# Optimization experiments

Measured on AMD Instinct MI355X. Metric: run time of the kernel, lower is better.

## Reference

```python
import jax, jax.numpy as jnp
import numpy as np

N_CELL, N_GENE, D, E = 100000, 20000, 128, 1000000


def setup_inputs() -> dict:
    key = jax.random.key(0)
    ks = jax.random.split(key, 16)
    return {
        "cell_z": jax.random.normal(ks[0], (N_CELL, D), jnp.float32),
        "gene_z": jax.random.normal(ks[1], (N_GENE, D), jnp.float32),
        "W_gene": jax.random.normal(ks[2], (D, D), jnp.float32) / np.sqrt(D),
        "b_gene": jax.random.normal(ks[3], (D,), jnp.float32) * 0.01,
        "cell_scale": jax.random.normal(ks[4], (N_CELL,), jnp.float32),
        "cell_bias": jax.random.normal(ks[5], (N_CELL,), jnp.float32),
        "cell_std": jax.random.uniform(ks[6], (N_CELL,), jnp.float32, 0.1, 1.0),
        "gene_scale": jax.random.normal(ks[7], (N_GENE,), jnp.float32),
        "gene_bias": jax.random.normal(ks[8], (N_GENE,), jnp.float32),
        "gene_std": jax.random.uniform(ks[9], (N_GENE,), jnp.float32, 0.1, 1.0),
        "src_idx": jax.random.randint(ks[10], (E,), 0, N_CELL, jnp.int32),
        "dst_idx": jax.random.randint(ks[11], (E,), 0, N_GENE, jnp.int32),
        "cell_n_id": jax.random.randint(ks[12], (N_CELL,), 0, N_CELL, jnp.int32),
        "gene_n_id": jax.random.randint(ks[13], (N_GENE,), 0, N_GENE, jnp.int32),
    }


def reference(cell_z, gene_z, W_gene, b_gene,
              cell_scale, cell_bias, cell_std,
              gene_scale, gene_bias, gene_std,
              src_idx, dst_idx, cell_n_id, gene_n_id):
    # Relation projection: 'cell' -> Identity, 'gene' -> Linear + LeakyReLU.
    # Project per-node then gather (mathematically identical to the original
    # gather-then-project since projection is pointwise per node).
    gene_proj = jax.nn.leaky_relu(gene_z @ W_gene + b_gene)  # [N_GENE, D]
    u = cell_z[src_idx]            # [E, D] gather of src node embeddings
    v = gene_proj[dst_idx]         # [E, D] gather of projected dst embeddings

    # Per-edge scale/bias/std lookups via global node ids (n_id[edge_index]).
    sid = cell_n_id[src_idx]       # [E]
    did = gene_n_id[dst_idx]       # [E]
    s_sc, s_b, s_sd = cell_scale[sid], cell_bias[sid], cell_std[sid]
    d_sc, d_b, d_sd = gene_scale[did], gene_bias[did], gene_std[did]

    dot = jnp.sum(u * v, axis=-1)  # [E]
    loc = dot * s_sc * d_sc + s_b + d_b
    std = s_sd * d_sd
    return jnp.stack([loc, std])   # [2, E]
```

## Files before the change

kernel.cpp:

```cpp
#include <hip/hip_runtime.h>

#define N_CELL 100000
#define N_GENE 20000
#define DIM    128
#define N_EDGE 1000000

#define NS_STRIPE 15
#define NTILE     45
#define NBLK_SORT 977

#define NB_CAST 6250
#define NB_HIST 977
#define NB_PROJ 1250
#define NB_CTAB 391
#define NB_GTAB 79
#define NB_PREP (NB_CAST + NB_HIST + NB_PROJ + NB_CTAB + NB_GTAB)

typedef float f32x4 __attribute__((ext_vector_type(4)));

__device__ inline unsigned short f2bf(float f) {
    unsigned u = __float_as_uint(f);
    u += 0x7fffu + ((u >> 16) & 1u);
    return (unsigned short)(u >> 16);
}

__device__ inline void dot2(float& acc, unsigned a, unsigned b) {
    asm("v_dot2_f32_bf16 %0, %1, %2, %0" : "+v"(acc) : "v"(a), "v"(b));
}

__device__ inline int tile_of(int s, int d) {
    const int ss = (int)(((long long)s * 161049LL) >> 30);
    const int ds = (int)(((long long)d * 161049LL) >> 30);
    return ds * NS_STRIPE + ss;
}

__global__ __launch_bounds__(256) void prep_kernel(
    const float* __restrict__ gene_z,
    const float* __restrict__ W,
    const float* __restrict__ b,
    ushort* __restrict__ gene_projb,
    const float* __restrict__ cell_z,
    ushort4* __restrict__ cell_zb4,
    const int*   __restrict__ src_idx,
    const int*   __restrict__ dst_idx,
    const int*   __restrict__ cell_n_id,
    const int*   __restrict__ gene_n_id,
    const float* __restrict__ cell_scale,
    const float* __restrict__ cell_bias,
    const float* __restrict__ cell_std,
    const float* __restrict__ gene_scale,
    const float* __restrict__ gene_bias,
    const float* __restrict__ gene_std,
    float4* __restrict__ cell_p4,
    float4* __restrict__ gene_p4,
    int* __restrict__ counts)
{
    __shared__ float zlds[16][DIM];

    const int tid = threadIdx.x;
    int blk = blockIdx.x;

    if (blk < NB_CAST) {
        const f32x4* in4 = (const f32x4*)cell_z;
        const int base = blk * 512 + tid;
        const f32x4 v0 = __builtin_nontemporal_load(in4 + base);
        const f32x4 v1 = __builtin_nontemporal_load(in4 + base + 256);
        ushort4 o0, o1;
        o0.x = f2bf(v0.x); o0.y = f2bf(v0.y); o0.z = f2bf(v0.z); o0.w = f2bf(v0.w);
        o1.x = f2bf(v1.x); o1.y = f2bf(v1.y); o1.z = f2bf(v1.z); o1.w = f2bf(v1.w);
        cell_zb4[base]       = o0;
        cell_zb4[base + 256] = o1;
        return;
    }
    blk -= NB_CAST;

    if (blk < NB_HIST) {
        if (!counts) return;
        int* lcnt = (int*)&zlds[0][0];
        if (tid < NTILE) lcnt[tid] = 0;
        __syncthreads();
        #pragma unroll
        for (int c = 0; c < 4; ++c) {
            const int e = blk * 1024 + c * 256 + tid;
            if (e < N_EDGE) {
                const int t = tile_of(src_idx[e], dst_idx[e]);
                atomicAdd(&lcnt[t], 1);
            }
        }
        __syncthreads();
        if (tid < NTILE) counts[tid * NBLK_SORT + blk] = lcnt[tid];
        return;
    }
    blk -= NB_HIST;

    if (blk < NB_PROJ) {
        const int row0 = blk * 16;
        const f32x4* Z4  = (const f32x4*)(gene_z + (long)row0 * DIM);
        f32x4*       zl4 = (f32x4*)&zlds[0][0];
        zl4[tid]       = __builtin_nontemporal_load(Z4 + tid);
        zl4[tid + 256] = __builtin_nontemporal_load(Z4 + tid + 256);
        __syncthreads();

        const int col   = tid & 127;
        const int rbase = (tid >> 7) * 8;

        const float bias = b[col];
        float acc[8];
        #pragma unroll
        for (int r = 0; r < 8; ++r) acc[r] = bias;

        #pragma unroll 8
        for (int k4 = 0; k4 < DIM / 4; ++k4) {
            float4 zv[8];
            #pragma unroll
            for (int r = 0; r < 8; ++r)
                zv[r] = ((const float4*)&zlds[rbase + r][0])[k4];
            #pragma unroll
            for (int kk = 0; kk < 4; ++kk) {
                const float w = W[(k4 * 4 + kk) * DIM + col];
                #pragma unroll
                for (int r = 0; r < 8; ++r) {
                    const float z = (kk == 0) ? zv[r].x : (kk == 1) ? zv[r].y
                                   : (kk == 2) ? zv[r].z : zv[r].w;
                    acc[r] = fmaf(z, w, acc[r]);
                }
            }
        }
        #pragma unroll
        for (int r = 0; r < 8; ++r) {
            const float v = acc[r];
            gene_projb[(long)(row0 + rbase + r) * DIM + col] =
                f2bf(v > 0.f ? v : 0.01f * v);
        }
        return;
    }
    blk -= NB_PROJ;

    if (blk < NB_CTAB) {
        if (!cell_p4) return;
        const int c = blk * 256 + tid;
        if (c < N_CELL) {
            const int id = cell_n_id[c];
            cell_p4[c] = make_float4(cell_scale[id], cell_bias[id],
                                     cell_std[id], 0.f);
        }
        return;
    }
    blk -= NB_CTAB;

    if (!gene_p4) return;
    const int g = blk * 256 + tid;
    if (g < N_GENE) {
        const int id = gene_n_id[g];
        gene_p4[g] = make_float4(gene_scale[id], gene_bias[id],
                                 gene_std[id], 0.f);
    }
}

__global__ __launch_bounds__(256) void scanA_kernel(
    int* __restrict__ counts, int* __restrict__ totals)
{
    __shared__ int sd[256];
    const int t   = blockIdx.x;
    const int tid = threadIdx.x;
    int carry = 0;
    for (int c = 0; c < 4; ++c) {
        const int idx = c * 256 + tid;
        const int val = (idx < NBLK_SORT) ? counts[t * NBLK_SORT + idx] : 0;
        sd[tid] = val;
        __syncthreads();
        #pragma unroll
        for (int off = 1; off < 256; off <<= 1) {
            const int tmp = (tid >= off) ? sd[tid - off] : 0;
            __syncthreads();
            sd[tid] += tmp;
            __syncthreads();
        }
        const int incl  = sd[tid];
        const int ctot  = sd[255];
        if (idx < NBLK_SORT) counts[t * NBLK_SORT + idx] = carry + incl - val;
        carry += ctot;
        __syncthreads();
    }
    if (tid == 0) totals[t] = carry;
}

__global__ void scanB_kernel(const int* __restrict__ totals,
                             int* __restrict__ bases)
{
    if (threadIdx.x == 0 && blockIdx.x == 0) {
        int s = 0;
        for (int i = 0; i < NTILE; ++i) { bases[i] = s; s += totals[i]; }
    }
}

__global__ __launch_bounds__(256) void scatter_kernel(
    const int* __restrict__ src_idx,
    const int* __restrict__ dst_idx,
    const int* __restrict__ counts,
    const int* __restrict__ bases,
    int2* __restrict__ sorted_sd,
    int*  __restrict__ sorted_e)
{
    __shared__ int lcnt[NTILE];
    __shared__ int lbase[NTILE];
    const int tid = threadIdx.x;
    const int blk = blockIdx.x;
    if (tid < NTILE) lcnt[tid] = 0;
    __syncthreads();

    int ts[4], rs[4], ss[4], ds[4], es[4];
    #pragma unroll
    for (int c = 0; c < 4; ++c) {
        const int e = blk * 1024 + c * 256 + tid;
        es[c] = e;
        if (e < N_EDGE) {
            ss[c] = src_idx[e];
            ds[c] = dst_idx[e];
            ts[c] = tile_of(ss[c], ds[c]);
            rs[c] = atomicAdd(&lcnt[ts[c]], 1);
        } else { ts[c] = -1; rs[c] = 0; ss[c] = 0; ds[c] = 0; }
    }
    __syncthreads();
    if (tid < NTILE) lbase[tid] = bases[tid] + counts[tid * NBLK_SORT + blk];
    __syncthreads();

    #pragma unroll
    for (int c = 0; c < 4; ++c) {
        if (ts[c] >= 0) {
            const int pos = lbase[ts[c]] + rs[c];
            sorted_sd[pos] = make_int2(ss[c], ds[c]);
            sorted_e[pos]  = es[c];
        }
    }
}

__global__ __launch_bounds__(256) void edge_sorted_kernel(
    const ushort* __restrict__ cell_zb,
    const ushort* __restrict__ gene_projb,
    const int2* __restrict__ sorted_sd,
    const int*  __restrict__ sorted_e,
    const float4* __restrict__ cell_p4,
    const float4* __restrict__ gene_p4,
    float* __restrict__ out)
{
    const int wg  = blockIdx.x;
    const int xcd = wg & 7;
    const int sub = wg >> 3;
    const int q = 15625 / 8, r = 15625 % 8;
    const int swz = ((xcd < r) ? xcd * (q + 1) : r * (q + 1) + (xcd - r) * q) + sub;

    const int tid  = threadIdx.x;
    const int lane = tid & 15;
    const int grp  = swz * 16 + (tid >> 4);

    const int4 p0 = ((const int4*)sorted_sd)[grp * 2];
    const int4 p1 = ((const int4*)sorted_sd)[grp * 2 + 1];
    const int4 e4 = ((const int4*)sorted_e)[grp];

    uint4 a0 = ((const uint4*)(cell_zb    + (long)p0.x * DIM))[lane];
    uint4 a1 = ((const uint4*)(cell_zb    + (long)p0.z * DIM))[lane];
    uint4 a2 = ((const uint4*)(cell_zb    + (long)p1.x * DIM))[lane];
    uint4 a3 = ((const uint4*)(cell_zb    + (long)p1.z * DIM))[lane];
    uint4 v0 = ((const uint4*)(gene_projb + (long)p0.y * DIM))[lane];
    uint4 v1 = ((const uint4*)(gene_projb + (long)p0.w * DIM))[lane];
    uint4 v2 = ((const uint4*)(gene_projb + (long)p1.y * DIM))[lane];
    uint4 v3 = ((const uint4*)(gene_projb + (long)p1.w * DIM))[lane];

    float dot0 = 0.f, dot1 = 0.f, dot2v = 0.f, dot3 = 0.f;
    dot2(dot0, a0.x, v0.x); dot2(dot0, a0.y, v0.y);
    dot2(dot0, a0.z, v0.z); dot2(dot0, a0.w, v0.w);
    dot2(dot1, a1.x, v1.x); dot2(dot1, a1.y, v1.y);
    dot2(dot1, a1.z, v1.z); dot2(dot1, a1.w, v1.w);
    dot2(dot2v, a2.x, v2.x); dot2(dot2v, a2.y, v2.y);
    dot2(dot2v, a2.z, v2.z); dot2(dot2v, a2.w, v2.w);
    dot2(dot3, a3.x, v3.x); dot2(dot3, a3.y, v3.y);
    dot2(dot3, a3.z, v3.z); dot2(dot3, a3.w, v3.w);

    #define RED(d)                 \
        d += __shfl_xor(d, 1);     \
        d += __shfl_xor(d, 2);     \
        d += __shfl_xor(d, 4);     \
        d += __shfl_xor(d, 8);
    RED(dot0) RED(dot1) RED(dot2v) RED(dot3)
    #undef RED

    if (lane < 4) {
        const float dj = (lane & 2) ? ((lane & 1) ? dot3 : dot2v)
                                    : ((lane & 1) ? dot1 : dot0);
        const int sj   = (lane & 2) ? ((lane & 1) ? p1.z : p1.x)
                                    : ((lane & 1) ? p0.z : p0.x);
        const int djx  = (lane & 2) ? ((lane & 1) ? p1.w : p1.y)
                                    : ((lane & 1) ? p0.w : p0.y);
        const int e    = (lane & 2) ? ((lane & 1) ? e4.w : e4.z)
                                    : ((lane & 1) ? e4.y : e4.x);
        const float4 cs = cell_p4[sj];
        const float4 gs = gene_p4[djx];
        out[e]          = dj * cs.x * gs.x + cs.y + gs.y;
        out[N_EDGE + e] = cs.z * gs.z;
    }
}

template<bool TAB>
__global__ __launch_bounds__(256) void edge_kernel(
    const ushort* __restrict__ cell_zb,
    const ushort* __restrict__ gene_projb,
    const int*   __restrict__ src_idx,
    const int*   __restrict__ dst_idx,
    const int*   __restrict__ cell_n_id,
    const int*   __restrict__ gene_n_id,
    const float* __restrict__ cell_scale,
    const float* __restrict__ cell_bias,
    const float* __restrict__ cell_std,
    const float* __restrict__ gene_scale,
    const float* __restrict__ gene_bias,
    const float* __restrict__ gene_std,
    const float4* __restrict__ cell_p4,
    const float4* __restrict__ gene_p4,
    float* __restrict__ out)
{
    const int tid  = threadIdx.x;
    const int lane = tid & 15;
    const int grp  = blockIdx.x * 16 + (tid >> 4);
    const int e0   = grp * 4;

    const int4 s4 = ((const int4*)src_idx)[grp];
    const int4 d4 = ((const int4*)dst_idx)[grp];

    uint4 a0 = ((const uint4*)(cell_zb    + (long)s4.x * DIM))[lane];
    uint4 a1 = ((const uint4*)(cell_zb    + (long)s4.y * DIM))[lane];
    uint4 a2 = ((const uint4*)(cell_zb    + (long)s4.z * DIM))[lane];
    uint4 a3 = ((const uint4*)(cell_zb    + (long)s4.w * DIM))[lane];
    uint4 v0 = ((const uint4*)(gene_projb + (long)d4.x * DIM))[lane];
    uint4 v1 = ((const uint4*)(gene_projb + (long)d4.y * DIM))[lane];
    uint4 v2 = ((const uint4*)(gene_projb + (long)d4.z * DIM))[lane];
    uint4 v3 = ((const uint4*)(gene_projb + (long)d4.w * DIM))[lane];

    float dot0 = 0.f, dot1 = 0.f, dot2v = 0.f, dot3 = 0.f;
    dot2(dot0, a0.x, v0.x); dot2(dot0, a0.y, v0.y);
    dot2(dot0, a0.z, v0.z); dot2(dot0, a0.w, v0.w);
    dot2(dot1, a1.x, v1.x); dot2(dot1, a1.y, v1.y);
    dot2(dot1, a1.z, v1.z); dot2(dot1, a1.w, v1.w);
    dot2(dot2v, a2.x, v2.x); dot2(dot2v, a2.y, v2.y);
    dot2(dot2v, a2.z, v2.z); dot2(dot2v, a2.w, v2.w);
    dot2(dot3, a3.x, v3.x); dot2(dot3, a3.y, v3.y);
    dot2(dot3, a3.z, v3.z); dot2(dot3, a3.w, v3.w);

    #define RED(d)                 \
        d += __shfl_xor(d, 1);     \
        d += __shfl_xor(d, 2);     \
        d += __shfl_xor(d, 4);     \
        d += __shfl_xor(d, 8);
    RED(dot0) RED(dot1) RED(dot2v) RED(dot3)
    #undef RED

    if (lane < 4) {
        const float dj = (lane & 2) ? ((lane & 1) ? dot3 : dot2v)
                                    : ((lane & 1) ? dot1 : dot0);
        const int sj   = (lane & 2) ? ((lane & 1) ? s4.w : s4.z)
                                    : ((lane & 1) ? s4.y : s4.x);
        const int djx  = (lane & 2) ? ((lane & 1) ? d4.w : d4.z)
                                    : ((lane & 1) ? d4.y : d4.x);
        float sc_s, b_s, sd_s, sc_d, b_d, sd_d;
        if (TAB) {
            const float4 cs = cell_p4[sj];
            const float4 gs = gene_p4[djx];
            sc_s = cs.x; b_s = cs.y; sd_s = cs.z;
            sc_d = gs.x; b_d = gs.y; sd_d = gs.z;
        } else {
            const int sid = cell_n_id[sj];
            const int did = gene_n_id[djx];
            sc_s = cell_scale[sid]; b_s = cell_bias[sid]; sd_s = cell_std[sid];
            sc_d = gene_scale[did]; b_d = gene_bias[did]; sd_d = gene_std[did];
        }
        const int e = e0 + lane;
        out[e]          = dj * sc_s * sc_d + b_s + b_d;
        out[N_EDGE + e] = sd_s * sd_d;
    }
}

extern "C" void kernel_launch(void* const* d_in, const int* in_sizes, int n_in,
                              void* d_out, int out_size, void* d_ws, size_t ws_size,
                              hipStream_t stream) {
    const float* cell_z     = (const float*)d_in[0];
    const float* gene_z     = (const float*)d_in[1];
    const float* W_gene     = (const float*)d_in[2];
    const float* b_gene     = (const float*)d_in[3];
    const float* cell_scale = (const float*)d_in[4];
    const float* cell_bias  = (const float*)d_in[5];
    const float* cell_std   = (const float*)d_in[6];
    const float* gene_scale = (const float*)d_in[7];
    const float* gene_bias  = (const float*)d_in[8];
    const float* gene_std   = (const float*)d_in[9];
    const int*   src_idx    = (const int*)d_in[10];
    const int*   dst_idx    = (const int*)d_in[11];
    const int*   cell_n_id  = (const int*)d_in[12];
    const int*   gene_n_id  = (const int*)d_in[13];

    char* ws = (char*)d_ws;
    size_t off = 0;
    ushort* gene_projb = (ushort*)(ws + off); off += (size_t)N_GENE * DIM * 2;
    ushort* cell_zb    = (ushort*)(ws + off); off += (size_t)N_CELL * DIM * 2;
    const size_t base_need = off;

    float4* cell_p4 = nullptr; float4* gene_p4 = nullptr;
    size_t off_tab = off;
    const size_t tab_need = (size_t)N_CELL * 16 + (size_t)N_GENE * 16;

    int2* sorted_sd = nullptr; int* sorted_e = nullptr;
    int* counts = nullptr; int* totals = nullptr; int* bases = nullptr;

    const size_t sort_need = (size_t)N_EDGE * 8 + (size_t)N_EDGE * 4
                           + (size_t)NTILE * NBLK_SORT * 4 + 512;

    const bool tab  = (ws_size >= base_need + tab_need);
    const bool srt  = tab && (ws_size >= base_need + tab_need + sort_need);

    if (tab) {
        cell_p4 = (float4*)(ws + off_tab);
        gene_p4 = (float4*)(ws + off_tab + (size_t)N_CELL * 16);
        off = off_tab + tab_need;
    }
    if (srt) {
        sorted_sd = (int2*)(ws + off); off += (size_t)N_EDGE * 8;
        sorted_e  = (int*)(ws + off);  off += (size_t)N_EDGE * 4;
        counts    = (int*)(ws + off);  off += (size_t)NTILE * NBLK_SORT * 4;
        totals    = (int*)(ws + off);  off += 256;
        bases     = (int*)(ws + off);  off += 256;
    }

    float* out = (float*)d_out;

    prep_kernel<<<NB_PREP, 256, 0, stream>>>(
        gene_z, W_gene, b_gene, gene_projb,
        cell_z, (ushort4*)cell_zb,
        src_idx, dst_idx, cell_n_id, gene_n_id,
        cell_scale, cell_bias, cell_std,
        gene_scale, gene_bias, gene_std,
        cell_p4, gene_p4, counts);

    if (srt) {
        scanA_kernel<<<NTILE, 256, 0, stream>>>(counts, totals);
        scanB_kernel<<<1, 64, 0, stream>>>(totals, bases);
        scatter_kernel<<<NBLK_SORT, 256, 0, stream>>>(
            src_idx, dst_idx, counts, bases, sorted_sd, sorted_e);
        edge_sorted_kernel<<<N_EDGE / 64, 256, 0, stream>>>(
            cell_zb, gene_projb, sorted_sd, sorted_e, cell_p4, gene_p4, out);
    } else if (tab) {
        edge_kernel<true><<<N_EDGE / 64, 256, 0, stream>>>(
            cell_zb, gene_projb, src_idx, dst_idx, cell_n_id, gene_n_id,
            cell_scale, cell_bias, cell_std, gene_scale, gene_bias, gene_std,
            cell_p4, gene_p4, out);
    } else {
        edge_kernel<false><<<N_EDGE / 64, 256, 0, stream>>>(
            cell_zb, gene_projb, src_idx, dst_idx, cell_n_id, gene_n_id,
            cell_scale, cell_bias, cell_std, gene_scale, gene_bias, gene_std,
            nullptr, nullptr, out);
    }
}
```

Measured before the change: 107.1 us.

## Pack sorted edge indices, write results in sorted order, add gather fixup pass

Edges are now bucketed into 20 source stripes by 2 destination halves, and each edge's source and destination are packed into one 32-bit word, which halves the sorted-index traffic. The edge kernel writes float2 results in sorted order, and a new fixup kernel gathers them back to original edge order through a rank array, so the output stores become coalesced. The one-thread base scan kernel is folded into the scatter kernel, removing a launch. The projection loop is restructured, and nontemporal loads are replaced with normal loads. In exchange there is an extra kernel launch plus an intermediate result buffer that is written and then read back with random gathers.

```diff
diff --git a/kernel.cpp b/kernel.cpp
--- a/kernel.cpp
+++ b/kernel.cpp
@@ -5,8 +5,9 @@
 #define DIM    128
 #define N_EDGE 1000000
 
-#define NS_STRIPE 15
-#define NTILE     45
+#define NS_STRIPE 20
+#define ND_STRIPE 2
+#define NTILE     40
 #define NBLK_SORT 977
 
 #define NB_CAST 6250
@@ -29,9 +30,13 @@
 }
 
 __device__ inline int tile_of(int s, int d) {
-    const int ss = (int)(((long long)s * 161049LL) >> 30);
-    const int ds = (int)(((long long)d * 161049LL) >> 30);
+    const int ss = (int)(((unsigned long long)s * 429497ULL) >> 31);
+    const int ds = (d >= 10000) ? 1 : 0;
     return ds * NS_STRIPE + ss;
+}
+
+__device__ inline unsigned pack_sd(int s, int d) {
+    return ((unsigned)s << 15) | (unsigned)d;
 }
 
 __global__ __launch_bounds__(256) void prep_kernel(
@@ -63,8 +68,8 @@
     if (blk < NB_CAST) {
         const f32x4* in4 = (const f32x4*)cell_z;
         const int base = blk * 512 + tid;
-        const f32x4 v0 = __builtin_nontemporal_load(in4 + base);
-        const f32x4 v1 = __builtin_nontemporal_load(in4 + base + 256);
+        const f32x4 v0 = in4[base];
+        const f32x4 v1 = in4[base + 256];
         ushort4 o0, o1;
         o0.x = f2bf(v0.x); o0.y = f2bf(v0.y); o0.z = f2bf(v0.z); o0.w = f2bf(v0.w);
         o1.x = f2bf(v1.x); o1.y = f2bf(v1.y); o1.z = f2bf(v1.z); o1.w = f2bf(v1.w);
@@ -97,8 +102,8 @@
         const int row0 = blk * 16;
         const f32x4* Z4  = (const f32x4*)(gene_z + (long)row0 * DIM);
         f32x4*       zl4 = (f32x4*)&zlds[0][0];
-        zl4[tid]       = __builtin_nontemporal_load(Z4 + tid);
-        zl4[tid + 256] = __builtin_nontemporal_load(Z4 + tid + 256);
+        zl4[tid]       = Z4[tid];
+        zl4[tid + 256] = Z4[tid + 256];
         __syncthreads();
 
         const int col   = tid & 127;
@@ -109,21 +114,19 @@
         #pragma unroll
         for (int r = 0; r < 8; ++r) acc[r] = bias;
 
-        #pragma unroll 8
         for (int k4 = 0; k4 < DIM / 4; ++k4) {
-            float4 zv[8];
+            const float w0 = W[(k4 * 4 + 0) * DIM + col];
+            const float w1 = W[(k4 * 4 + 1) * DIM + col];
+            const float w2 = W[(k4 * 4 + 2) * DIM + col];
+            const float w3 = W[(k4 * 4 + 3) * DIM + col];
             #pragma unroll
-            for (int r = 0; r < 8; ++r)
-                zv[r] = ((const float4*)&zlds[rbase + r][0])[k4];
-            #pragma unroll
-            for (int kk = 0; kk < 4; ++kk) {
-                const float w = W[(k4 * 4 + kk) * DIM + col];
-                #pragma unroll
-                for (int r = 0; r < 8; ++r) {
-                    const float z = (kk == 0) ? zv[r].x : (kk == 1) ? zv[r].y
-                                   : (kk == 2) ? zv[r].z : zv[r].w;
-                    acc[r] = fmaf(z, w, acc[r]);
-                }
+            for (int rp = 0; rp < 4; ++rp) {
+                const float4 za = ((const float4*)&zlds[rbase + 2*rp][0])[k4];
+                const float4 zb = ((const float4*)&zlds[rbase + 2*rp + 1][0])[k4];
+                acc[2*rp]     = fmaf(za.x, w0, fmaf(za.y, w1,
+                                fmaf(za.z, w2, fmaf(za.w, w3, acc[2*rp]))));
+                acc[2*rp + 1] = fmaf(zb.x, w0, fmaf(zb.y, w1,
+                                fmaf(zb.z, w2, fmaf(zb.w, w3, acc[2*rp + 1]))));
             }
         }
         #pragma unroll
@@ -176,44 +179,35 @@
             sd[tid] += tmp;
             __syncthreads();
         }
-        const int incl  = sd[tid];
-        const int ctot  = sd[255];
+        const int incl = sd[tid];
+        const int ctot = sd[255];
         if (idx < NBLK_SORT) counts[t * NBLK_SORT + idx] = carry + incl - val;
         carry += ctot;
         __syncthreads();
     }
     if (tid == 0) totals[t] = carry;
-}
-
-__global__ void scanB_kernel(const int* __restrict__ totals,
-                             int* __restrict__ bases)
-{
-    if (threadIdx.x == 0 && blockIdx.x == 0) {
-        int s = 0;
-        for (int i = 0; i < NTILE; ++i) { bases[i] = s; s += totals[i]; }
-    }
 }
 
 __global__ __launch_bounds__(256) void scatter_kernel(
     const int* __restrict__ src_idx,
     const int* __restrict__ dst_idx,
     const int* __restrict__ counts,
-    const int* __restrict__ bases,
-    int2* __restrict__ sorted_sd,
-    int*  __restrict__ sorted_e)
+    const int* __restrict__ totals,
+    unsigned* __restrict__ sorted_p,
+    int*      __restrict__ rank)
 {
     __shared__ int lcnt[NTILE];
+    __shared__ int sbase[NTILE];
     __shared__ int lbase[NTILE];
     const int tid = threadIdx.x;
     const int blk = blockIdx.x;
     if (tid < NTILE) lcnt[tid] = 0;
     __syncthreads();
 
-    int ts[4], rs[4], ss[4], ds[4], es[4];
+    int ts[4], rs[4], ss[4], ds[4];
     #pragma unroll
     for (int c = 0; c < 4; ++c) {
         const int e = blk * 1024 + c * 256 + tid;
-        es[c] = e;
         if (e < N_EDGE) {
             ss[c] = src_idx[e];
             ds[c] = dst_idx[e];
@@ -222,15 +216,21 @@
         } else { ts[c] = -1; rs[c] = 0; ss[c] = 0; ds[c] = 0; }
     }
     __syncthreads();
-    if (tid < NTILE) lbase[tid] = bases[tid] + counts[tid * NBLK_SORT + blk];
+    if (tid == 0) {
+        int s = 0;
+        for (int i = 0; i < NTILE; ++i) { sbase[i] = s; s += totals[i]; }
+    }
+    __syncthreads();
+    if (tid < NTILE) lbase[tid] = sbase[tid] + counts[tid * NBLK_SORT + blk];
     __syncthreads();
 
     #pragma unroll
     for (int c = 0; c < 4; ++c) {
+        const int e = blk * 1024 + c * 256 + tid;
         if (ts[c] >= 0) {
             const int pos = lbase[ts[c]] + rs[c];
-            sorted_sd[pos] = make_int2(ss[c], ds[c]);
-            sorted_e[pos]  = es[c];
+            sorted_p[pos] = pack_sd(ss[c], ds[c]);
+            rank[e] = pos;
         }
     }
 }
@@ -238,11 +238,10 @@
 __global__ __launch_bounds__(256) void edge_sorted_kernel(
     const ushort* __restrict__ cell_zb,
     const ushort* __restrict__ gene_projb,
-    const int2* __restrict__ sorted_sd,
-    const int*  __restrict__ sorted_e,
+    const unsigned* __restrict__ sorted_p,
     const float4* __restrict__ cell_p4,
     const float4* __restrict__ gene_p4,
-    float* __restrict__ out)
+    float2* __restrict__ res)
 {
     const int wg  = blockIdx.x;
     const int xcd = wg & 7;
@@ -254,18 +253,20 @@
     const int lane = tid & 15;
     const int grp  = swz * 16 + (tid >> 4);
 
-    const int4 p0 = ((const int4*)sorted_sd)[grp * 2];
-    const int4 p1 = ((const int4*)sorted_sd)[grp * 2 + 1];
-    const int4 e4 = ((const int4*)sorted_e)[grp];
-
-    uint4 a0 = ((const uint4*)(cell_zb    + (long)p0.x * DIM))[lane];
-    uint4 a1 = ((const uint4*)(cell_zb    + (long)p0.z * DIM))[lane];
-    uint4 a2 = ((const uint4*)(cell_zb    + (long)p1.x * DIM))[lane];
-    uint4 a3 = ((const uint4*)(cell_zb    + (long)p1.z * DIM))[lane];
-    uint4 v0 = ((const uint4*)(gene_projb + (long)p0.y * DIM))[lane];
-    uint4 v1 = ((const uint4*)(gene_projb + (long)p0.w * DIM))[lane];
-    uint4 v2 = ((const uint4*)(gene_projb + (long)p1.y * DIM))[lane];
-    uint4 v3 = ((const uint4*)(gene_projb + (long)p1.w * DIM))[lane];
+    const uint4 p = ((const uint4*)sorted_p)[grp];
+    const int s0 = (int)(p.x >> 15), d0 = (int)(p.x & 0x7fffu);
+    const int s1 = (int)(p.y >> 15), d1 = (int)(p.y & 0x7fffu);
+    const int s2 = (int)(p.z >> 15), d2 = (int)(p.z & 0x7fffu);
+    const int s3 = (int)(p.w >> 15), d3 = (int)(p.w & 0x7fffu);
+
+    uint4 a0 = ((const uint4*)(cell_zb    + (long)s0 * DIM))[lane];
+    uint4 a1 = ((const uint4*)(cell_zb    + (long)s1 * DIM))[lane];
+    uint4 a2 = ((const uint4*)(cell_zb    + (long)s2 * DIM))[lane];
+    uint4 a3 = ((const uint4*)(cell_zb    + (long)s3 * DIM))[lane];
+    uint4 v0 = ((const uint4*)(gene_projb + (long)d0 * DIM))[lane];
+    uint4 v1 = ((const uint4*)(gene_projb + (long)d1 * DIM))[lane];
+    uint4 v2 = ((const uint4*)(gene_projb + (long)d2 * DIM))[lane];
+    uint4 v3 = ((const uint4*)(gene_projb + (long)d3 * DIM))[lane];
 
     float dot0 = 0.f, dot1 = 0.f, dot2v = 0.f, dot3 = 0.f;
     dot2(dot0, a0.x, v0.x); dot2(dot0, a0.y, v0.y);
@@ -288,17 +289,31 @@
     if (lane < 4) {
         const float dj = (lane & 2) ? ((lane & 1) ? dot3 : dot2v)
                                     : ((lane & 1) ? dot1 : dot0);
-        const int sj   = (lane & 2) ? ((lane & 1) ? p1.z : p1.x)
-                                    : ((lane & 1) ? p0.z : p0.x);
-        const int djx  = (lane & 2) ? ((lane & 1) ? p1.w : p1.y)
-                                    : ((lane & 1) ? p0.w : p0.y);
-        const int e    = (lane & 2) ? ((lane & 1) ? e4.w : e4.z)
-                                    : ((lane & 1) ? e4.y : e4.x);
+        const int sj   = (lane & 2) ? ((lane & 1) ? s3 : s2)
+                                    : ((lane & 1) ? s1 : s0);
+        const int djx  = (lane & 2) ? ((lane & 1) ? d3 : d2)
+                                    : ((lane & 1) ? d1 : d0);
         const float4 cs = cell_p4[sj];
         const float4 gs = gene_p4[djx];
-        out[e]          = dj * cs.x * gs.x + cs.y + gs.y;
-        out[N_EDGE + e] = cs.z * gs.z;
-    }
+        res[grp * 4 + lane] =
+            make_float2(dj * cs.x * gs.x + cs.y + gs.y, cs.z * gs.z);
+    }
+}
+
+__global__ __launch_bounds__(256) void fixup_kernel(
+    const int*    __restrict__ rank,
+    const float2* __restrict__ res,
+    float* __restrict__ out)
+{
+    const int e0 = (blockIdx.x * 256 + threadIdx.x) * 4;
+    if (e0 >= N_EDGE) return;
+    const int4 r4 = *(const int4*)(rank + e0);
+    const float2 r0 = res[r4.x];
+    const float2 r1 = res[r4.y];
+    const float2 r2 = res[r4.z];
+    const float2 r3 = res[r4.w];
+    *(float4*)(out + e0)          = make_float4(r0.x, r1.x, r2.x, r3.x);
+    *(float4*)(out + N_EDGE + e0) = make_float4(r0.y, r1.y, r2.y, r3.y);
 }
 
 template<bool TAB>
@@ -407,14 +422,15 @@
     size_t off_tab = off;
     const size_t tab_need = (size_t)N_CELL * 16 + (size_t)N_GENE * 16;
 
-    int2* sorted_sd = nullptr; int* sorted_e = nullptr;
-    int* counts = nullptr; int* totals = nullptr; int* bases = nullptr;
-
-    const size_t sort_need = (size_t)N_EDGE * 8 + (size_t)N_EDGE * 4
-                           + (size_t)NTILE * NBLK_SORT * 4 + 512;
-
-    const bool tab  = (ws_size >= base_need + tab_need);
-    const bool srt  = tab && (ws_size >= base_need + tab_need + sort_need);
+    unsigned* sorted_p = nullptr; int* rank = nullptr; float2* res = nullptr;
+    int* counts = nullptr; int* totals = nullptr;
+    const size_t sort_need = (size_t)N_EDGE * 4
+                           + (size_t)N_EDGE * 4
+                           + (size_t)N_EDGE * 8
+                           + (size_t)NTILE * NBLK_SORT * 4 + 256;
+
+    const bool tab = (ws_size >= base_need + tab_need);
+    const bool srt = tab && (ws_size >= base_need + tab_need + sort_need);
 
     if (tab) {
         cell_p4 = (float4*)(ws + off_tab);
@@ -422,11 +438,11 @@
         off = off_tab + tab_need;
     }
     if (srt) {
-        sorted_sd = (int2*)(ws + off); off += (size_t)N_EDGE * 8;
-        sorted_e  = (int*)(ws + off);  off += (size_t)N_EDGE * 4;
-        counts    = (int*)(ws + off);  off += (size_t)NTILE * NBLK_SORT * 4;
-        totals    = (int*)(ws + off);  off += 256;
-        bases     = (int*)(ws + off);  off += 256;
+        sorted_p = (unsigned*)(ws + off); off += (size_t)N_EDGE * 4;
+        rank     = (int*)(ws + off);      off += (size_t)N_EDGE * 4;
+        res      = (float2*)(ws + off);   off += (size_t)N_EDGE * 8;
+        counts   = (int*)(ws + off);      off += (size_t)NTILE * NBLK_SORT * 4;
+        totals   = (int*)(ws + off);      off += 256;
     }
 
     float* out = (float*)d_out;
@@ -441,11 +457,11 @@
 
     if (srt) {
         scanA_kernel<<<NTILE, 256, 0, stream>>>(counts, totals);
-        scanB_kernel<<<1, 64, 0, stream>>>(totals, bases);
         scatter_kernel<<<NBLK_SORT, 256, 0, stream>>>(
-            src_idx, dst_idx, counts, bases, sorted_sd, sorted_e);
+            src_idx, dst_idx, counts, totals, sorted_p, rank);
         edge_sorted_kernel<<<N_EDGE / 64, 256, 0, stream>>>(
-            cell_zb, gene_projb, sorted_sd, sorted_e, cell_p4, gene_p4, out);
+            cell_zb, gene_projb, sorted_p, cell_p4, gene_p4, res);
+        fixup_kernel<<<(N_EDGE / 4 + 255) / 256, 256, 0, stream>>>(rank, res, out);
     } else if (tab) {
         edge_kernel<true><<<N_EDGE / 64, 256, 0, stream>>>(
             cell_zb, gene_projb, src_idx, dst_idx, cell_n_id, gene_n_id,
```

New measurement: 87.16 us. -18.6%, faster.
